# Kernel optimization log

Measured on AMD Instinct MI355X. Metric: run time of the kernel, lower is better.

Reference implementation:

```python
import jax, jax.numpy as jnp
import numpy as np

N_NODES = 100000
N_EDGES = 1200000
D_IN = 64
D_HID = 64
D_OUT = 32


def setup_inputs() -> dict:
    key = jax.random.key(0)
    ks = jax.random.split(key, 8)
    x = jax.random.normal(ks[0], (N_NODES, D_IN), dtype=jnp.float32)
    edge_index = jax.random.randint(ks[1], (2, N_EDGES), 0, N_NODES, dtype=jnp.int64)
    s = 0.05
    W1 = jax.random.normal(ks[2], (D_IN, D_HID), dtype=jnp.float32) * s
    b1 = jnp.zeros((D_HID,), dtype=jnp.float32)
    W2 = jax.random.normal(ks[3], (D_HID, D_HID), dtype=jnp.float32) * s
    b2 = jnp.zeros((D_HID,), dtype=jnp.float32)
    Wl = jax.random.normal(ks[4], (D_HID, D_OUT), dtype=jnp.float32) * s
    bl = jax.random.normal(ks[5], (D_OUT,), dtype=jnp.float32) * s
    return {"x": x, "edge_index": edge_index, "W1": W1, "b1": b1,
            "W2": W2, "b2": b2, "Wl": Wl, "bl": bl}


def reference(x, edge_index, W1, b1, W2, b2, Wl, bl):
    n = x.shape[0]
    # PyG GCNConv default: add self-loops, symmetric normalization D^-1/2 (A+I) D^-1/2
    loops = jnp.arange(n, dtype=edge_index.dtype)
    src = jnp.concatenate([edge_index[0], loops])  # message sources
    dst = jnp.concatenate([edge_index[1], loops])  # aggregation targets
    deg = jax.ops.segment_sum(jnp.ones(dst.shape, x.dtype), dst, num_segments=n)
    dinv = jax.lax.rsqrt(deg)  # deg >= 1 due to self-loops
    norm = dinv[src] * dinv[dst]  # [E+N]

    def gcn_conv(h, W, b):
        h = h @ W                      # transform [N, d]
        m = h[src] * norm[:, None]     # gather + scale [E+N, d]
        return jax.ops.segment_sum(m, dst, num_segments=n) + b  # scatter-add

    h = jax.nn.relu(gcn_conv(x, W1, b1))
    h = jax.nn.relu(gcn_conv(h, W2, b2))
    return h @ Wl + bl
```

## Files before the change

### kernel.cpp

```cpp
#include <hip/hip_runtime.h>
#include <hip/hip_fp16.h>

#define N_NODES 100000
#define N_EDGES 1200000

#define BIN_SHIFT 6
#define NODES_PER_BIN 64
#define NBINS ((N_NODES + NODES_PER_BIN - 1) >> BIN_SHIFT)
#define CAP 1024
#define EPB 8192
#define NBLK_BIN ((N_EDGES + EPB - 1) / EPB)
#define NBLK_GEMM ((N_NODES + 63) / 64)
#define SMEM_BYTES 55424

__global__ __launch_bounds__(256, 2) void bin_gemm1_kernel(
    const int* __restrict__ src, const int* __restrict__ dst,
    int* __restrict__ gcursor, unsigned int* __restrict__ binned,
    const float* __restrict__ X, const float* __restrict__ W1,
    __half* __restrict__ tmp) {
    __shared__ __align__(16) char smem[SMEM_BYTES];
    int t = threadIdx.x;

    if (blockIdx.x < NBLK_BIN) {
        unsigned int* stage = (unsigned int*)smem;
        unsigned short* sbin = (unsigned short*)(smem + EPB * 4);
        unsigned int* hist = (unsigned int*)(smem + EPB * 4 + EPB * 2);
        int e_base = blockIdx.x * EPB;

        for (int b = t; b < NBINS; b += 256) hist[b] = 0;
        __syncthreads();

#pragma unroll
        for (int j = 0; j < EPB / 256; ++j) {
            int idx = e_base + t + j * 256;
            if (idx < N_EDGES) {
                int s = src[idx];
                int d = dst[idx];
                unsigned int bin = (unsigned int)d >> BIN_SHIFT;
                stage[t + j * 256] = (unsigned int)s | (((unsigned int)d & 63u) << 17);
                sbin[t + j * 256] = (unsigned short)bin;
                atomicAdd(&hist[bin], 1u);
            }
        }
        __syncthreads();

        for (int b = t; b < NBINS; b += 256) {
            unsigned int c = hist[b];
            if (c) hist[b] = (unsigned int)(b * CAP) + (unsigned int)atomicAdd(&gcursor[b], (int)c);
        }
        __syncthreads();

#pragma unroll
        for (int j = 0; j < EPB / 256; ++j) {
            int idx = e_base + t + j * 256;
            if (idx < N_EDGES) {
                unsigned int bin = sbin[t + j * 256];
                unsigned int pos = atomicAdd(&hist[bin], 1u);
                binned[pos] = stage[t + j * 256];
            }
        }
    } else {
        constexpr int COLG = 16, RGS = 16, RPT = 4, XPITCH = 17;
        float4* sW4 = (float4*)smem;
        float4* sX4 = (float4*)(smem + 64 * COLG * 16);

        for (int i = t; i < 64 * COLG; i += 256) sW4[i] = ((const float4*)W1)[i];

        int base_row = (blockIdx.x - NBLK_BIN) * 64;
        const float4* X4 = (const float4*)X;
        for (int i = t; i < 64 * 16; i += 256) {
            int r = i >> 4, c = i & 15;
            int gr = base_row + r;
            float4 v = make_float4(0.f, 0.f, 0.f, 0.f);
            if (gr < N_NODES) v = X4[(size_t)gr * 16 + c];
            sX4[r * XPITCH + c] = v;
        }
        __syncthreads();

        int cg = t % COLG;
        int rg = t / COLG;
        float4 acc[RPT];
#pragma unroll
        for (int r = 0; r < RPT; ++r) acc[r] = make_float4(0.f, 0.f, 0.f, 0.f);

#pragma unroll 2
        for (int k4 = 0; k4 < 16; ++k4) {
            float4 xv[RPT];
#pragma unroll
            for (int r = 0; r < RPT; ++r) xv[r] = sX4[(rg + RGS * r) * XPITCH + k4];
#pragma unroll
            for (int kk = 0; kk < 4; ++kk) {
                float4 w = sW4[(k4 * 4 + kk) * COLG + cg];
#pragma unroll
                for (int r = 0; r < RPT; ++r) {
                    float xs = (kk == 0) ? xv[r].x : (kk == 1) ? xv[r].y : (kk == 2) ? xv[r].z : xv[r].w;
                    acc[r].x = fmaf(xs, w.x, acc[r].x);
                    acc[r].y = fmaf(xs, w.y, acc[r].y);
                    acc[r].z = fmaf(xs, w.z, acc[r].z);
                    acc[r].w = fmaf(xs, w.w, acc[r].w);
                }
            }
        }

#pragma unroll
        for (int r = 0; r < RPT; ++r) {
            int grow = base_row + rg + RGS * r;
            if (grow < N_NODES) {
                float4 v = acc[r];
                __half2* H2 = (__half2*)tmp;
                size_t idx = (size_t)grow * 32 + 2 * cg;
                H2[idx]     = __floats2half2_rn(v.x, v.y);
                H2[idx + 1] = __floats2half2_rn(v.z, v.w);
            }
        }
    }
}

__global__ void csr_kernel(unsigned int* __restrict__ binned,
                           const int* __restrict__ gcursor,
                           float* __restrict__ dinv,
                           unsigned int* __restrict__ offdeg) {
    __shared__ unsigned int eLDS[CAP];
    __shared__ unsigned int counts[NODES_PER_BIN];
    __shared__ unsigned int scan[NODES_PER_BIN];
    __shared__ unsigned int offs[NODES_PER_BIN];
    __shared__ unsigned int cur[NODES_PER_BIN];
    int bin = blockIdx.x;
    int t = threadIdx.x;
    int nb = gcursor[bin];
    unsigned int* eb = binned + (size_t)bin * CAP;

    if (t < NODES_PER_BIN) counts[t] = 0;
    __syncthreads();
    for (int i = t; i < nb; i += 256) {
        unsigned int p = eb[i];
        eLDS[i] = p;
        atomicAdd(&counts[p >> 17], 1u);
    }
    __syncthreads();
    if (t < NODES_PER_BIN) scan[t] = counts[t];
    __syncthreads();
    for (int step = 1; step < NODES_PER_BIN; step <<= 1) {
        unsigned int v = 0;
        if (t < NODES_PER_BIN && t >= step) v = scan[t - step];
        __syncthreads();
        if (t < NODES_PER_BIN) scan[t] += v;
        __syncthreads();
    }
    if (t < NODES_PER_BIN) {
        offs[t] = scan[t] - counts[t];
        cur[t] = 0;
    }
    __syncthreads();
    for (int i = t; i < nb; i += 256) {
        unsigned int p = eLDS[i];
        unsigned int l = p >> 17;
        unsigned int pos = offs[l] + atomicAdd(&cur[l], 1u);
        eb[pos] = p & 0x1FFFFu;
    }
    if (t < NODES_PER_BIN) {
        int node = bin * NODES_PER_BIN + t;
        if (node < N_NODES) {
            dinv[node] = rsqrtf((float)(counts[t] + 1u));
            offdeg[node] = (offs[t] << 16) | counts[t];
        }
    }
}

template<int DOUT, bool HALF_OUT, bool ROWSCALE, bool GEMM_BIAS, bool PRESCALED>
__global__ __launch_bounds__(256, 6) void fused_agg_gemm(
    const __half* __restrict__ tmp,
    const unsigned int* __restrict__ binned,
    const int* __restrict__ gcursor,
    const unsigned int* __restrict__ offdeg,
    const float* __restrict__ dinv,
    const float* __restrict__ gb,
    const float* __restrict__ W,
    const float* __restrict__ gbias,
    void* __restrict__ Hout) {
    constexpr int COLG = DOUT / 4;
    constexpr int RGS  = 256 / COLG;
    constexpr int RPT  = 64 / RGS;
    constexpr int XPITCH = 17;
    __shared__ unsigned int srcs[CAP];
    __shared__ unsigned int sOffdeg[NODES_PER_BIN];
    __shared__ float sDinv[NODES_PER_BIN];
    __shared__ float4 sH4[64 * XPITCH];

    int bin = blockIdx.x;
    int t = threadIdx.x;
    int nb = gcursor[bin];
    const unsigned int* eb = binned + (size_t)bin * CAP;

    if (t < NODES_PER_BIN) {
        int node = bin * NODES_PER_BIN + t;
        sOffdeg[t] = (node < N_NODES) ? offdeg[node] : 0;
        sDinv[t]   = (node < N_NODES) ? dinv[node]   : 0.0f;
    }
    for (int i = t; i < nb; i += 256) srcs[i] = eb[i];
    __syncthreads();

    int oct = t & 7;
    int lnode0 = t >> 3;
    const uint4* tmp16 = (const uint4*)tmp;
    float bb[8];
    {
        const float4 b0 = ((const float4*)gb)[oct * 2];
        const float4 b1 = ((const float4*)gb)[oct * 2 + 1];
        bb[0] = b0.x; bb[1] = b0.y; bb[2] = b0.z; bb[3] = b0.w;
        bb[4] = b1.x; bb[5] = b1.y; bb[6] = b1.z; bb[7] = b1.w;
    }

#pragma unroll
    for (int g = 0; g < 2; ++g) {
        int ln = g * 32 + lnode0;
        int node = bin * NODES_PER_BIN + ln;
        if (node < N_NODES) {
            unsigned int od = sOffdeg[ln];
            int deg = (int)(od & 0xFFFFu);
            int beg = (int)(od >> 16);
            float dv = sDinv[ln];
            float acc[8];
            {
                uint4 raw = tmp16[(size_t)node * 8 + oct];
                const __half2* hp = (const __half2*)&raw;
                float selfs = PRESCALED ? 1.0f : dv;
#pragma unroll
                for (int j = 0; j < 4; ++j) {
                    float2 f = __half22float2(hp[j]);
                    acc[2 * j] = selfs * f.x; acc[2 * j + 1] = selfs * f.y;
                }
            }
            int e = 0;
            for (; e + 3 < deg; e += 4) {
                unsigned int s0 = srcs[beg + e];
                unsigned int s1 = srcs[beg + e + 1];
                unsigned int s2 = srcs[beg + e + 2];
                unsigned int s3 = srcs[beg + e + 3];
                float w0 = 1.f, w1 = 1.f, w2 = 1.f, w3 = 1.f;
                if (!PRESCALED) {
                    w0 = dinv[s0]; w1 = dinv[s1]; w2 = dinv[s2]; w3 = dinv[s3];
                }
                uint4 r0 = tmp16[(size_t)s0 * 8 + oct];
                uint4 r1 = tmp16[(size_t)s1 * 8 + oct];
                uint4 r2 = tmp16[(size_t)s2 * 8 + oct];
                uint4 r3 = tmp16[(size_t)s3 * 8 + oct];
                const __half2* h0 = (const __half2*)&r0;
                const __half2* h1 = (const __half2*)&r1;
                const __half2* h2 = (const __half2*)&r2;
                const __half2* h3 = (const __half2*)&r3;
#pragma unroll
                for (int j = 0; j < 4; ++j) {
                    float2 f0 = __half22float2(h0[j]);
                    float2 f1 = __half22float2(h1[j]);
                    float2 f2 = __half22float2(h2[j]);
                    float2 f3 = __half22float2(h3[j]);
                    if (PRESCALED) {
                        acc[2 * j]     += (f0.x + f1.x) + (f2.x + f3.x);
                        acc[2 * j + 1] += (f0.y + f1.y) + (f2.y + f3.y);
                    } else {
                        acc[2 * j]     = fmaf(w0, f0.x, fmaf(w1, f1.x, fmaf(w2, f2.x, fmaf(w3, f3.x, acc[2 * j]))));
                        acc[2 * j + 1] = fmaf(w0, f0.y, fmaf(w1, f1.y, fmaf(w2, f2.y, fmaf(w3, f3.y, acc[2 * j + 1]))));
                    }
                }
            }
            for (; e < deg; ++e) {
                unsigned int s0 = srcs[beg + e];
                float w0 = PRESCALED ? 1.0f : dinv[s0];
                uint4 r0 = tmp16[(size_t)s0 * 8 + oct];
                const __half2* h0 = (const __half2*)&r0;
#pragma unroll
                for (int j = 0; j < 4; ++j) {
                    float2 f0 = __half22float2(h0[j]);
                    acc[2 * j]     = fmaf(w0, f0.x, acc[2 * j]);
                    acc[2 * j + 1] = fmaf(w0, f0.y, acc[2 * j + 1]);
                }
            }
            float4 o0, o1;
            o0.x = fmaxf(fmaf(dv, acc[0], bb[0]), 0.0f);
            o0.y = fmaxf(fmaf(dv, acc[1], bb[1]), 0.0f);
            o0.z = fmaxf(fmaf(dv, acc[2], bb[2]), 0.0f);
            o0.w = fmaxf(fmaf(dv, acc[3], bb[3]), 0.0f);
            o1.x = fmaxf(fmaf(dv, acc[4], bb[4]), 0.0f);
            o1.y = fmaxf(fmaf(dv, acc[5], bb[5]), 0.0f);
            o1.z = fmaxf(fmaf(dv, acc[6], bb[6]), 0.0f);
            o1.w = fmaxf(fmaf(dv, acc[7], bb[7]), 0.0f);
            sH4[ln * XPITCH + oct * 2]     = o0;
            sH4[ln * XPITCH + oct * 2 + 1] = o1;
        }
    }
    __syncthreads();

    int cg = t % COLG;
    int rg = t / COLG;
    const float4* W4 = (const float4*)W;
    float4 acc[RPT];
#pragma unroll
    for (int r = 0; r < RPT; ++r) acc[r] = make_float4(0.f, 0.f, 0.f, 0.f);

#pragma unroll 2
    for (int k4 = 0; k4 < 16; ++k4) {
        float4 xv[RPT];
#pragma unroll
        for (int r = 0; r < RPT; ++r) xv[r] = sH4[(rg + RGS * r) * XPITCH + k4];
#pragma unroll
        for (int kk = 0; kk < 4; ++kk) {
            float4 w = W4[(k4 * 4 + kk) * COLG + cg];
#pragma unroll
            for (int r = 0; r < RPT; ++r) {
                float xs = (kk == 0) ? xv[r].x : (kk == 1) ? xv[r].y : (kk == 2) ? xv[r].z : xv[r].w;
                acc[r].x = fmaf(xs, w.x, acc[r].x);
                acc[r].y = fmaf(xs, w.y, acc[r].y);
                acc[r].z = fmaf(xs, w.z, acc[r].z);
                acc[r].w = fmaf(xs, w.w, acc[r].w);
            }
        }
    }

#pragma unroll
    for (int r = 0; r < RPT; ++r) {
        int ln = rg + RGS * r;
        int node = bin * NODES_PER_BIN + ln;
        if (node < N_NODES) {
            float4 v = acc[r];
            if (ROWSCALE) {
                float s = sDinv[ln];
                v.x *= s; v.y *= s; v.z *= s; v.w *= s;
            }
            if (GEMM_BIAS) {
                float4 bbq = ((const float4*)gbias)[cg];
                v.x += bbq.x; v.y += bbq.y; v.z += bbq.z; v.w += bbq.w;
            }
            if (HALF_OUT) {
                __half2* H2 = (__half2*)Hout;
                size_t idx = (size_t)node * (DOUT / 2) + 2 * cg;
                H2[idx]     = __floats2half2_rn(v.x, v.y);
                H2[idx + 1] = __floats2half2_rn(v.z, v.w);
            } else {
                ((float4*)Hout)[(size_t)node * COLG + cg] = v;
            }
        }
    }
}

extern "C" void kernel_launch(void* const* d_in, const int* in_sizes, int n_in,
                              void* d_out, int out_size, void* d_ws, size_t ws_size,
                              hipStream_t stream) {
    const float* x  = (const float*)d_in[0];
    const int*   ei = (const int*)d_in[1];
    const float* W1 = (const float*)d_in[2];
    const float* b1 = (const float*)d_in[3];
    const float* W2 = (const float*)d_in[4];
    const float* b2 = (const float*)d_in[5];
    const float* Wl = (const float*)d_in[6];
    const float* bl = (const float*)d_in[7];
    float* out = (float*)d_out;

    const int* src = ei;
    const int* dst = ei + N_EDGES;

    char* ws = (char*)d_ws;
    size_t off = 0;
    auto align = [](size_t v) { return (v + 511) & ~(size_t)511; };
    int* gcursor         = (int*)(ws + off);          off = align(off + (size_t)NBINS * 4);
    float* dinv          = (float*)(ws + off);        off = align(off + (size_t)N_NODES * 4);
    unsigned int* offdeg = (unsigned int*)(ws + off); off = align(off + (size_t)N_NODES * 4);
    unsigned int* binned = (unsigned int*)(ws + off); off = align(off + (size_t)NBINS * CAP * 4);
    __half* tmp          = (__half*)(ws + off);       off = align(off + (size_t)N_NODES * 64 * 2);
    __half* tmp2         = (__half*)(ws + off);       off = align(off + (size_t)N_NODES * 64 * 2);
    (void)ws_size;

    hipMemsetAsync(gcursor, 0, (size_t)NBINS * 4, stream);
    bin_gemm1_kernel<<<NBLK_BIN + NBLK_GEMM, 256, 0, stream>>>(
        src, dst, gcursor, binned, x, W1, tmp);

    csr_kernel<<<NBINS, 256, 0, stream>>>(binned, gcursor, dinv, offdeg);

    fused_agg_gemm<64, true, true, false, false><<<NBINS, 256, 0, stream>>>(
        tmp, binned, gcursor, offdeg, dinv, b1, W2, nullptr, tmp2);

    fused_agg_gemm<32, false, false, true, true><<<NBINS, 256, 0, stream>>>(
        tmp2, binned, gcursor, offdeg, dinv, b2, Wl, bl, out);
}
```

Measured before the change: 190.0 us.

## Fuse CSR build into first aggregation kernel, compute degrees via global histogram

Removes the separate csr_kernel launch by folding the per-bin counting sort into the first aggregate+GEMM kernel, which sorts into LDS and writes the result back for the second layer. Node degrees needed for neighbour normalisation now come from a new global atomic histogram over dst, run as extra blocks of the binning kernel, and dinv is recomputed with rsqrt on the fly instead of being stored. This saves one launch and one global round trip of the binned edges. The cost is extra global atomics, extra degree gathers with rsqrt per edge, and a write-back of the sorted lists.

```diff
diff --git a/kernel.cpp b/kernel.cpp
--- a/kernel.cpp
+++ b/kernel.cpp
@@ -13,9 +13,10 @@
 #define NBLK_GEMM ((N_NODES + 63) / 64)
 #define SMEM_BYTES 55424
 
-__global__ __launch_bounds__(256, 2) void bin_gemm1_kernel(
+__global__ __launch_bounds__(256, 2) void bin_gemm1_hist_kernel(
     const int* __restrict__ src, const int* __restrict__ dst,
-    int* __restrict__ gcursor, unsigned int* __restrict__ binned,
+    int* __restrict__ gcursor, int* __restrict__ degs,
+    unsigned int* __restrict__ binned,
     const float* __restrict__ X, const float* __restrict__ W1,
     __half* __restrict__ tmp) {
     __shared__ __align__(16) char smem[SMEM_BYTES];
@@ -59,7 +60,7 @@
                 binned[pos] = stage[t + j * 256];
             }
         }
-    } else {
+    } else if (blockIdx.x < NBLK_BIN + NBLK_GEMM) {
         constexpr int COLG = 16, RGS = 16, RPT = 4, XPITCH = 17;
         float4* sW4 = (float4*)smem;
         float4* sX4 = (float4*)(smem + 64 * COLG * 16);
@@ -113,22 +114,38 @@
                 H2[idx + 1] = __floats2half2_rn(v.z, v.w);
             }
         }
+    } else {
+        int e_base = (blockIdx.x - NBLK_BIN - NBLK_GEMM) * EPB;
+#pragma unroll
+        for (int j = 0; j < EPB / 256; ++j) {
+            int idx = e_base + t + j * 256;
+            if (idx < N_EDGES) atomicAdd(&degs[dst[idx]], 1);
+        }
     }
 }
 
-__global__ void csr_kernel(unsigned int* __restrict__ binned,
-                           const int* __restrict__ gcursor,
-                           float* __restrict__ dinv,
-                           unsigned int* __restrict__ offdeg) {
-    __shared__ unsigned int eLDS[CAP];
+__global__ __launch_bounds__(256, 6) void fused1_kernel(
+    const __half* __restrict__ tmp,
+    unsigned int* __restrict__ binned,
+    const int* __restrict__ gcursor,
+    const int* __restrict__ degs,
+    const float* __restrict__ gb,
+    const float* __restrict__ W,
+    unsigned int* __restrict__ offdeg,
+    __half* __restrict__ tmp2) {
+    constexpr int COLG = 16, RGS = 16, RPT = 4, XPITCH = 17;
+    __shared__ unsigned int srcs[CAP];
     __shared__ unsigned int counts[NODES_PER_BIN];
     __shared__ unsigned int scan[NODES_PER_BIN];
     __shared__ unsigned int offs[NODES_PER_BIN];
     __shared__ unsigned int cur[NODES_PER_BIN];
+    __shared__ float4 sH4[64 * XPITCH];
+
     int bin = blockIdx.x;
     int t = threadIdx.x;
     int nb = gcursor[bin];
     unsigned int* eb = binned + (size_t)bin * CAP;
+    unsigned int* eLDS = (unsigned int*)sH4;
 
     if (t < NODES_PER_BIN) counts[t] = 0;
     __syncthreads();
@@ -156,49 +173,14 @@
         unsigned int p = eLDS[i];
         unsigned int l = p >> 17;
         unsigned int pos = offs[l] + atomicAdd(&cur[l], 1u);
-        eb[pos] = p & 0x1FFFFu;
-    }
+        srcs[pos] = p & 0x1FFFFu;
+    }
+    __syncthreads();
+    for (int i = t; i < nb; i += 256) eb[i] = srcs[i];
     if (t < NODES_PER_BIN) {
         int node = bin * NODES_PER_BIN + t;
-        if (node < N_NODES) {
-            dinv[node] = rsqrtf((float)(counts[t] + 1u));
-            offdeg[node] = (offs[t] << 16) | counts[t];
-        }
-    }
-}
-
-template<int DOUT, bool HALF_OUT, bool ROWSCALE, bool GEMM_BIAS, bool PRESCALED>
-__global__ __launch_bounds__(256, 6) void fused_agg_gemm(
-    const __half* __restrict__ tmp,
-    const unsigned int* __restrict__ binned,
-    const int* __restrict__ gcursor,
-    const unsigned int* __restrict__ offdeg,
-    const float* __restrict__ dinv,
-    const float* __restrict__ gb,
-    const float* __restrict__ W,
-    const float* __restrict__ gbias,
-    void* __restrict__ Hout) {
-    constexpr int COLG = DOUT / 4;
-    constexpr int RGS  = 256 / COLG;
-    constexpr int RPT  = 64 / RGS;
-    constexpr int XPITCH = 17;
-    __shared__ unsigned int srcs[CAP];
-    __shared__ unsigned int sOffdeg[NODES_PER_BIN];
-    __shared__ float sDinv[NODES_PER_BIN];
-    __shared__ float4 sH4[64 * XPITCH];
-
-    int bin = blockIdx.x;
-    int t = threadIdx.x;
-    int nb = gcursor[bin];
-    const unsigned int* eb = binned + (size_t)bin * CAP;
-
-    if (t < NODES_PER_BIN) {
-        int node = bin * NODES_PER_BIN + t;
-        sOffdeg[t] = (node < N_NODES) ? offdeg[node] : 0;
-        sDinv[t]   = (node < N_NODES) ? dinv[node]   : 0.0f;
-    }
-    for (int i = t; i < nb; i += 256) srcs[i] = eb[i];
-    __syncthreads();
+        if (node < N_NODES) offdeg[node] = (offs[t] << 16) | counts[t];
+    }
 
     int oct = t & 7;
     int lnode0 = t >> 3;
@@ -206,9 +188,9 @@
     float bb[8];
     {
         const float4 b0 = ((const float4*)gb)[oct * 2];
-        const float4 b1 = ((const float4*)gb)[oct * 2 + 1];
+        const float4 b1v = ((const float4*)gb)[oct * 2 + 1];
         bb[0] = b0.x; bb[1] = b0.y; bb[2] = b0.z; bb[3] = b0.w;
-        bb[4] = b1.x; bb[5] = b1.y; bb[6] = b1.z; bb[7] = b1.w;
+        bb[4] = b1v.x; bb[5] = b1v.y; bb[6] = b1v.z; bb[7] = b1v.w;
     }
 
 #pragma unroll
@@ -216,19 +198,17 @@
         int ln = g * 32 + lnode0;
         int node = bin * NODES_PER_BIN + ln;
         if (node < N_NODES) {
-            unsigned int od = sOffdeg[ln];
-            int deg = (int)(od & 0xFFFFu);
-            int beg = (int)(od >> 16);
-            float dv = sDinv[ln];
+            int deg = (int)counts[ln];
+            int beg = (int)offs[ln];
+            float dv = rsqrtf((float)(deg + 1));
             float acc[8];
             {
                 uint4 raw = tmp16[(size_t)node * 8 + oct];
                 const __half2* hp = (const __half2*)&raw;
-                float selfs = PRESCALED ? 1.0f : dv;
 #pragma unroll
                 for (int j = 0; j < 4; ++j) {
                     float2 f = __half22float2(hp[j]);
-                    acc[2 * j] = selfs * f.x; acc[2 * j + 1] = selfs * f.y;
+                    acc[2 * j] = dv * f.x; acc[2 * j + 1] = dv * f.y;
                 }
             }
             int e = 0;
@@ -237,10 +217,10 @@
                 unsigned int s1 = srcs[beg + e + 1];
                 unsigned int s2 = srcs[beg + e + 2];
                 unsigned int s3 = srcs[beg + e + 3];
-                float w0 = 1.f, w1 = 1.f, w2 = 1.f, w3 = 1.f;
-                if (!PRESCALED) {
-                    w0 = dinv[s0]; w1 = dinv[s1]; w2 = dinv[s2]; w3 = dinv[s3];
-                }
+                float w0 = rsqrtf((float)(degs[s0] + 1));
+                float w1 = rsqrtf((float)(degs[s1] + 1));
+                float w2 = rsqrtf((float)(degs[s2] + 1));
+                float w3 = rsqrtf((float)(degs[s3] + 1));
                 uint4 r0 = tmp16[(size_t)s0 * 8 + oct];
                 uint4 r1 = tmp16[(size_t)s1 * 8 + oct];
                 uint4 r2 = tmp16[(size_t)s2 * 8 + oct];
@@ -255,18 +235,13 @@
                     float2 f1 = __half22float2(h1[j]);
                     float2 f2 = __half22float2(h2[j]);
                     float2 f3 = __half22float2(h3[j]);
-                    if (PRESCALED) {
-                        acc[2 * j]     += (f0.x + f1.x) + (f2.x + f3.x);
-                        acc[2 * j + 1] += (f0.y + f1.y) + (f2.y + f3.y);
-                    } else {
-                        acc[2 * j]     = fmaf(w0, f0.x, fmaf(w1, f1.x, fmaf(w2, f2.x, fmaf(w3, f3.x, acc[2 * j]))));
-                        acc[2 * j + 1] = fmaf(w0, f0.y, fmaf(w1, f1.y, fmaf(w2, f2.y, fmaf(w3, f3.y, acc[2 * j + 1]))));
-                    }
+                    acc[2 * j]     = fmaf(w0, f0.x, fmaf(w1, f1.x, fmaf(w2, f2.x, fmaf(w3, f3.x, acc[2 * j]))));
+                    acc[2 * j + 1] = fmaf(w0, f0.y, fmaf(w1, f1.y, fmaf(w2, f2.y, fmaf(w3, f3.y, acc[2 * j + 1]))));
                 }
             }
             for (; e < deg; ++e) {
                 unsigned int s0 = srcs[beg + e];
-                float w0 = PRESCALED ? 1.0f : dinv[s0];
+                float w0 = rsqrtf((float)(degs[s0] + 1));
                 uint4 r0 = tmp16[(size_t)s0 * 8 + oct];
                 const __half2* h0 = (const __half2*)&r0;
 #pragma unroll
@@ -322,23 +297,158 @@
         int ln = rg + RGS * r;
         int node = bin * NODES_PER_BIN + ln;
         if (node < N_NODES) {
+            float s = rsqrtf((float)(counts[ln] + 1));
             float4 v = acc[r];
-            if (ROWSCALE) {
-                float s = sDinv[ln];
-                v.x *= s; v.y *= s; v.z *= s; v.w *= s;
-            }
-            if (GEMM_BIAS) {
-                float4 bbq = ((const float4*)gbias)[cg];
-                v.x += bbq.x; v.y += bbq.y; v.z += bbq.z; v.w += bbq.w;
-            }
-            if (HALF_OUT) {
-                __half2* H2 = (__half2*)Hout;
-                size_t idx = (size_t)node * (DOUT / 2) + 2 * cg;
-                H2[idx]     = __floats2half2_rn(v.x, v.y);
-                H2[idx + 1] = __floats2half2_rn(v.z, v.w);
-            } else {
-                ((float4*)Hout)[(size_t)node * COLG + cg] = v;
-            }
+            v.x *= s; v.y *= s; v.z *= s; v.w *= s;
+            __half2* H2 = (__half2*)tmp2;
+            size_t idx = (size_t)node * 32 + 2 * cg;
+            H2[idx]     = __floats2half2_rn(v.x, v.y);
+            H2[idx + 1] = __floats2half2_rn(v.z, v.w);
+        }
+    }
+}
+
+__global__ __launch_bounds__(256, 6) void fused2_kernel(
+    const __half* __restrict__ tmp2,
+    const unsigned int* __restrict__ binned,
+    const int* __restrict__ gcursor,
+    const unsigned int* __restrict__ offdeg,
+    const float* __restrict__ gb,
+    const float* __restrict__ W,
+    const float* __restrict__ gbias,
+    float* __restrict__ out) {
+    constexpr int COLG = 8, RGS = 32, RPT = 2, XPITCH = 17;
+    __shared__ unsigned int srcs[CAP];
+    __shared__ unsigned int sOffdeg[NODES_PER_BIN];
+    __shared__ float4 sH4[64 * XPITCH];
+
+    int bin = blockIdx.x;
+    int t = threadIdx.x;
+    int nb = gcursor[bin];
+    const unsigned int* eb = binned + (size_t)bin * CAP;
+
+    if (t < NODES_PER_BIN) {
+        int node = bin * NODES_PER_BIN + t;
+        sOffdeg[t] = (node < N_NODES) ? offdeg[node] : 0;
+    }
+    for (int i = t; i < nb; i += 256) srcs[i] = eb[i];
+    __syncthreads();
+
+    int oct = t & 7;
+    int lnode0 = t >> 3;
+    const uint4* tmp16 = (const uint4*)tmp2;
+    float bb[8];
+    {
+        const float4 b0 = ((const float4*)gb)[oct * 2];
+        const float4 b1v = ((const float4*)gb)[oct * 2 + 1];
+        bb[0] = b0.x; bb[1] = b0.y; bb[2] = b0.z; bb[3] = b0.w;
+        bb[4] = b1v.x; bb[5] = b1v.y; bb[6] = b1v.z; bb[7] = b1v.w;
+    }
+
+#pragma unroll
+    for (int g = 0; g < 2; ++g) {
+        int ln = g * 32 + lnode0;
+        int node = bin * NODES_PER_BIN + ln;
+        if (node < N_NODES) {
+            unsigned int od = sOffdeg[ln];
+            int deg = (int)(od & 0xFFFFu);
+            int beg = (int)(od >> 16);
+            float dv = rsqrtf((float)(deg + 1));
+            float acc[8];
+            {
+                uint4 raw = tmp16[(size_t)node * 8 + oct];
+                const __half2* hp = (const __half2*)&raw;
+#pragma unroll
+                for (int j = 0; j < 4; ++j) {
+                    float2 f = __half22float2(hp[j]);
+                    acc[2 * j] = f.x; acc[2 * j + 1] = f.y;
+                }
+            }
+            int e = 0;
+            for (; e + 3 < deg; e += 4) {
+                unsigned int s0 = srcs[beg + e];
+                unsigned int s1 = srcs[beg + e + 1];
+                unsigned int s2 = srcs[beg + e + 2];
+                unsigned int s3 = srcs[beg + e + 3];
+                uint4 r0 = tmp16[(size_t)s0 * 8 + oct];
+                uint4 r1 = tmp16[(size_t)s1 * 8 + oct];
+                uint4 r2 = tmp16[(size_t)s2 * 8 + oct];
+                uint4 r3 = tmp16[(size_t)s3 * 8 + oct];
+                const __half2* h0 = (const __half2*)&r0;
+                const __half2* h1 = (const __half2*)&r1;
+                const __half2* h2 = (const __half2*)&r2;
+                const __half2* h3 = (const __half2*)&r3;
+#pragma unroll
+                for (int j = 0; j < 4; ++j) {
+                    float2 f0 = __half22float2(h0[j]);
+                    float2 f1 = __half22float2(h1[j]);
+                    float2 f2 = __half22float2(h2[j]);
+                    float2 f3 = __half22float2(h3[j]);
+                    acc[2 * j]     += (f0.x + f1.x) + (f2.x + f3.x);
+                    acc[2 * j + 1] += (f0.y + f1.y) + (f2.y + f3.y);
+                }
+            }
+            for (; e < deg; ++e) {
+                unsigned int s0 = srcs[beg + e];
+                uint4 r0 = tmp16[(size_t)s0 * 8 + oct];
+                const __half2* h0 = (const __half2*)&r0;
+#pragma unroll
+                for (int j = 0; j < 4; ++j) {
+                    float2 f0 = __half22float2(h0[j]);
+                    acc[2 * j]     += f0.x;
+                    acc[2 * j + 1] += f0.y;
+                }
+            }
+            float4 o0, o1;
+            o0.x = fmaxf(fmaf(dv, acc[0], bb[0]), 0.0f);
+            o0.y = fmaxf(fmaf(dv, acc[1], bb[1]), 0.0f);
+            o0.z = fmaxf(fmaf(dv, acc[2], bb[2]), 0.0f);
+            o0.w = fmaxf(fmaf(dv, acc[3], bb[3]), 0.0f);
+            o1.x = fmaxf(fmaf(dv, acc[4], bb[4]), 0.0f);
+            o1.y = fmaxf(fmaf(dv, acc[5], bb[5]), 0.0f);
+            o1.z = fmaxf(fmaf(dv, acc[6], bb[6]), 0.0f);
+            o1.w = fmaxf(fmaf(dv, acc[7], bb[7]), 0.0f);
+            sH4[ln * XPITCH + oct * 2]     = o0;
+            sH4[ln * XPITCH + oct * 2 + 1] = o1;
+        }
+    }
+    __syncthreads();
+
+    int cg = t % COLG;
+    int rg = t / COLG;
+    const float4* W4 = (const float4*)W;
+    float4 acc[RPT];
+#pragma unroll
+    for (int r = 0; r < RPT; ++r) acc[r] = make_float4(0.f, 0.f, 0.f, 0.f);
+
+#pragma unroll 2
+    for (int k4 = 0; k4 < 16; ++k4) {
+        float4 xv[RPT];
+#pragma unroll
+        for (int r = 0; r < RPT; ++r) xv[r] = sH4[(rg + RGS * r) * XPITCH + k4];
+#pragma unroll
+        for (int kk = 0; kk < 4; ++kk) {
+            float4 w = W4[(k4 * 4 + kk) * COLG + cg];
+#pragma unroll
+            for (int r = 0; r < RPT; ++r) {
+                float xs = (kk == 0) ? xv[r].x : (kk == 1) ? xv[r].y : (kk == 2) ? xv[r].z : xv[r].w;
+                acc[r].x = fmaf(xs, w.x, acc[r].x);
+                acc[r].y = fmaf(xs, w.y, acc[r].y);
+                acc[r].z = fmaf(xs, w.z, acc[r].z);
+                acc[r].w = fmaf(xs, w.w, acc[r].w);
+            }
+        }
+    }
+
+#pragma unroll
+    for (int r = 0; r < RPT; ++r) {
+        int ln = rg + RGS * r;
+        int node = bin * NODES_PER_BIN + ln;
+        if (node < N_NODES) {
+            float4 v = acc[r];
+            float4 bbq = ((const float4*)gbias)[cg];
+            v.x += bbq.x; v.y += bbq.y; v.z += bbq.z; v.w += bbq.w;
+            ((float4*)out)[(size_t)node * COLG + cg] = v;
         }
     }
 }
@@ -362,23 +472,19 @@
     char* ws = (char*)d_ws;
     size_t off = 0;
     auto align = [](size_t v) { return (v + 511) & ~(size_t)511; };
-    int* gcursor         = (int*)(ws + off);          off = align(off + (size_t)NBINS * 4);
-    float* dinv          = (float*)(ws + off);        off = align(off + (size_t)N_NODES * 4);
+    int* gcursor         = (int*)(ws + off);          off += (size_t)NBINS * 4;
+    int* degs            = (int*)(ws + off);          off = align(off + (size_t)N_NODES * 4);
     unsigned int* offdeg = (unsigned int*)(ws + off); off = align(off + (size_t)N_NODES * 4);
     unsigned int* binned = (unsigned int*)(ws + off); off = align(off + (size_t)NBINS * CAP * 4);
     __half* tmp          = (__half*)(ws + off);       off = align(off + (size_t)N_NODES * 64 * 2);
     __half* tmp2         = (__half*)(ws + off);       off = align(off + (size_t)N_NODES * 64 * 2);
     (void)ws_size;
 
-    hipMemsetAsync(gcursor, 0, (size_t)NBINS * 4, stream);
-    bin_gemm1_kernel<<<NBLK_BIN + NBLK_GEMM, 256, 0, stream>>>(
-        src, dst, gcursor, binned, x, W1, tmp);
-
-    csr_kernel<<<NBINS, 256, 0, stream>>>(binned, gcursor, dinv, offdeg);
-
-    fused_agg_gemm<64, true, true, false, false><<<NBINS, 256, 0, stream>>>(
-        tmp, binned, gcursor, offdeg, dinv, b1, W2, nullptr, tmp2);
-
-    fused_agg_gemm<32, false, false, true, true><<<NBINS, 256, 0, stream>>>(
-        tmp2, binned, gcursor, offdeg, dinv, b2, Wl, bl, out);
+    hipMemsetAsync(gcursor, 0, (size_t)(NBINS + N_NODES) * 4, stream);
+    bin_gemm1_hist_kernel<<<NBLK_BIN + NBLK_GEMM + NBLK_BIN, 256, 0, stream>>>(
+        src, dst, gcursor, degs, binned, x, W1, tmp);
+
+    fused1_kernel<<<NBINS, 256, 0, stream>>>(tmp, binned, gcursor, degs, b1, W2, offdeg, tmp2);
+
+    fused2_kernel<<<NBINS, 256, 0, stream>>>(tmp2, binned, gcursor, offdeg, b2, Wl, bl, out);
 }
```

Result: slower. 236.4 us (+24.5%).
